# Kernel optimization log

Measured on AMD Instinct MI355X. Metric: run time of the kernel, lower is better.

Reference implementation:

```python
import jax, jax.numpy as jnp
import numpy as np

N = 50000
E = 500000
IN_C = 128
HEADS = 4
OUT_C = 64
EDGE_DIM = 32
NEG_SLOPE = 0.2  # PyG GATv2Conv default


def setup_inputs() -> dict:
    key = jax.random.key(0)
    ks = jax.random.split(key, 10)
    x = jax.random.normal(ks[0], (N, IN_C), dtype=jnp.float32)
    edge_index = jax.random.randint(ks[1], (2, E), 0, N, dtype=jnp.int64)
    edge_attr = jax.random.normal(ks[2], (E, EDGE_DIM), dtype=jnp.float32)
    s = 1.0 / np.sqrt(IN_C)
    W_l = jax.random.normal(ks[3], (IN_C, HEADS * OUT_C), dtype=jnp.float32) * s
    b_l = jnp.zeros((HEADS * OUT_C,), dtype=jnp.float32)
    W_r = jax.random.normal(ks[4], (IN_C, HEADS * OUT_C), dtype=jnp.float32) * s
    b_r = jnp.zeros((HEADS * OUT_C,), dtype=jnp.float32)
    W_e = jax.random.normal(ks[5], (EDGE_DIM, HEADS * OUT_C), dtype=jnp.float32) / np.sqrt(EDGE_DIM)
    att = jax.random.normal(ks[6], (HEADS, OUT_C), dtype=jnp.float32) / np.sqrt(OUT_C)
    bias = jnp.zeros((OUT_C,), dtype=jnp.float32)
    return {"x": x, "edge_index": edge_index, "edge_attr": edge_attr,
            "W_l": W_l, "b_l": b_l, "W_r": W_r, "b_r": b_r,
            "W_e": W_e, "att": att, "bias": bias}


def reference(x, edge_index, edge_attr, W_l, b_l, W_r, b_r, W_e, att, bias):
    # GATv2Conv forward (eval mode: dropout inactive), concat=False -> mean over heads
    src, dst = edge_index[0], edge_index[1]  # edge j -> i (source_to_target)
    x_l = (x @ W_l + b_l).reshape(N, HEADS, OUT_C)  # source transform
    x_r = (x @ W_r + b_r).reshape(N, HEADS, OUT_C)  # target transform
    e = (edge_attr @ W_e).reshape(E, HEADS, OUT_C)
    # per-edge score: att . LeakyReLU(x_l[j] + x_r[i] + e)
    m = x_l[src] + x_r[dst] + e                      # [E, H, C]
    m = jnp.where(m > 0, m, NEG_SLOPE * m)
    alpha = jnp.einsum('ehc,hc->eh', m, att)         # [E, H]
    # softmax over incoming edges of each target node
    amax = jax.ops.segment_max(alpha, dst, num_segments=N)   # [N, H]
    alpha = jnp.exp(alpha - amax[dst])
    denom = jax.ops.segment_sum(alpha, dst, num_segments=N)  # [N, H]
    alpha = alpha / denom[dst]
    # scatter-add weighted source messages
    out = jax.ops.segment_sum(alpha[:, :, None] * x_l[src], dst, num_segments=N)  # [N, H, C]
    out = out.mean(axis=1) + bias                    # concat=False -> mean heads
    return out
```

## Files before the change

kernel.cpp:

```cpp
#include <hip/hip_runtime.h>
#include <cstddef>

#define Nn 50000
#define Ee 500000
#define INC 128
#define HC 256
#define OUTC 64
#define EDIM 32
#define NEG 0.2f
#define NB 196
#define GEMMB 782

typedef __attribute__((ext_vector_type(8))) short short8;
typedef __attribute__((ext_vector_type(4))) float f32x4;

__device__ __forceinline__ unsigned short f2bf(float f) {
    unsigned u = __float_as_uint(f);
    return (unsigned short)((u + 0x7FFFu + ((u >> 16) & 1u)) >> 16);
}
__device__ __forceinline__ float bf2f(unsigned short v) {
    return __uint_as_float(((unsigned)v) << 16);
}

__device__ __forceinline__ float row_sum16(float x) {
    int i;
    i = __builtin_amdgcn_mov_dpp(__float_as_int(x), 0xB1, 0xF, 0xF, true);
    x += __int_as_float(i);
    i = __builtin_amdgcn_mov_dpp(__float_as_int(x), 0x4E, 0xF, 0xF, true);
    x += __int_as_float(i);
    i = __builtin_amdgcn_mov_dpp(__float_as_int(x), 0x141, 0xF, 0xF, true);
    x += __int_as_float(i);
    i = __builtin_amdgcn_mov_dpp(__float_as_int(x), 0x140, 0xF, 0xF, true);
    x += __int_as_float(i);
    return x;
}

__global__ __launch_bounds__(256) void pack_kernel(
    const float* __restrict__ Wl, const float* __restrict__ Wr,
    const float* __restrict__ We,
    unsigned short* __restrict__ wlf, unsigned short* __restrict__ wrf,
    unsigned short* __restrict__ wef, int* __restrict__ deg)
{
    int sid = blockIdx.x * 256 + threadIdx.x;
    if (sid >= 9216) {
        int i = sid - 9216;
        if (i < Nn) deg[i] = 0;
        return;
    }
    const float* W; unsigned short* dst; int s; int col; int k0;
    if (sid < 8192) {
        if (sid < 4096) { W = Wl; dst = wlf; s = sid; }
        else            { W = Wr; dst = wrf; s = sid - 4096; }
        int lane = s & 63;
        int T    = (s >> 6) & 15;
        int kc   = s >> 10;
        col = (lane & 15) * 16 + T;
        k0  = kc * 32 + (lane >> 4) * 8;
    } else {
        W = We; dst = wef; s = sid - 8192;
        int lane = s & 63;
        int nt   = (s >> 6) & 3;
        int cb   = s >> 8;
        col = cb * 64 + (lane & 15) * 4 + nt;
        k0  = (lane >> 4) * 8;
    }
    unsigned short tmp[8];
    #pragma unroll
    for (int j = 0; j < 8; ++j) tmp[j] = f2bf(W[(size_t)(k0 + j) * HC + col]);
    *(uint4*)(dst + (size_t)s * 8) = *(uint4*)tmp;
}

__global__ __launch_bounds__(256) void gemm_hist_kernel(
    const float* __restrict__ X,
    const unsigned short* __restrict__ wlf, const float* __restrict__ bl,
    const unsigned short* __restrict__ wrf, const float* __restrict__ br,
    unsigned short* __restrict__ Ylb, unsigned short* __restrict__ Yrb,
    const int* __restrict__ ei, int* __restrict__ deg)
{
    if (blockIdx.x >= GEMMB) {
        int e = (blockIdx.x - GEMMB) * 256 + threadIdx.x;
        if (e < Ee) atomicAdd(deg + ei[Ee + e], 1);
        return;
    }

    const int tid = threadIdx.x, lane = tid & 63;
    const int l15 = lane & 15, l4 = lane >> 4;
    const int r0 = blockIdx.x * 64 + (tid >> 6) * 16;

    int arow = r0 + l15; if (arow >= Nn) arow = Nn - 1;
    short8 af[4];
    #pragma unroll
    for (int kc = 0; kc < 4; ++kc) {
        const f32x4* p = (const f32x4*)(X + (size_t)arow * INC + kc * 32 + l4 * 8);
        f32x4 v0 = p[0], v1 = p[1];
        short8 a;
        a[0]=(short)f2bf(v0.x); a[1]=(short)f2bf(v0.y); a[2]=(short)f2bf(v0.z); a[3]=(short)f2bf(v0.w);
        a[4]=(short)f2bf(v1.x); a[5]=(short)f2bf(v1.y); a[6]=(short)f2bf(v1.z); a[7]=(short)f2bf(v1.w);
        af[kc] = a;
    }

    #pragma unroll 1
    for (int w = 0; w < 2; ++w) {
        const unsigned short* wf = w ? wrf : wlf;
        const float* b = w ? br : bl;
        unsigned short* Yb = w ? Yrb : Ylb;

        f32x4 acc[16];
        #pragma unroll
        for (int T = 0; T < 16; ++T) acc[T] = (f32x4){0.f, 0.f, 0.f, 0.f};

        #pragma unroll
        for (int kc = 0; kc < 4; ++kc) {
            #pragma unroll
            for (int T = 0; T < 16; ++T) {
                short8 bf = *(const short8*)(wf + ((size_t)(kc * 16 + T) * 64 + lane) * 8);
                acc[T] = __builtin_amdgcn_mfma_f32_16x16x32_bf16(af[kc], bf, acc[T], 0, 0, 0);
            }
        }

        float bb[16];
        #pragma unroll
        for (int t4 = 0; t4 < 4; ++t4) {
            float4 v = *(const float4*)(b + l15 * 16 + t4 * 4);
            bb[t4*4+0]=v.x; bb[t4*4+1]=v.y; bb[t4*4+2]=v.z; bb[t4*4+3]=v.w;
        }

        #pragma unroll
        for (int r = 0; r < 4; ++r) {
            int orow = r0 + l4 * 4 + r;
            if (orow < Nn) {
                unsigned short o[16];
                #pragma unroll
                for (int T = 0; T < 16; ++T) o[T] = f2bf(acc[T][r] + bb[T]);
                *(uint4*)(Yb + (size_t)orow * HC + l15 * 16)     = *(uint4*)(o);
                *(uint4*)(Yb + (size_t)orow * HC + l15 * 16 + 8) = *(uint4*)(o + 8);
            }
        }
    }
}

__global__ __launch_bounds__(256) void scan1_kernel(
    const int* __restrict__ deg, int* __restrict__ off, int* __restrict__ bsum) {
    __shared__ int s[256];
    int i = blockIdx.x * 256 + threadIdx.x;
    int v = (i < Nn) ? deg[i] : 0;
    s[threadIdx.x] = v;
    __syncthreads();
    #pragma unroll
    for (int d = 1; d < 256; d <<= 1) {
        int t = (threadIdx.x >= d) ? s[threadIdx.x - d] : 0;
        __syncthreads();
        s[threadIdx.x] += t;
        __syncthreads();
    }
    if (i < Nn) off[i] = s[threadIdx.x] - v;
    if (threadIdx.x == 255) bsum[blockIdx.x] = s[255];
}
__global__ __launch_bounds__(256) void scan3_kernel(
    int* __restrict__ off, const int* __restrict__ bsum, int* __restrict__ cur) {
    __shared__ int s[256];
    int t = threadIdx.x;
    int v = (t < NB) ? bsum[t] : 0;
    s[t] = v;
    __syncthreads();
    #pragma unroll
    for (int d = 1; d < 256; d <<= 1) {
        int tv = (t >= d) ? s[t - d] : 0;
        __syncthreads();
        s[t] += tv;
        __syncthreads();
    }
    int base = (blockIdx.x == 0) ? 0 : s[blockIdx.x - 1];
    int i = blockIdx.x * 256 + t;
    if (i < Nn) {
        int o = off[i] + base;
        off[i] = o;
        cur[i] = o;
    }
}
__global__ __launch_bounds__(256) void scatter_kernel(
    const int* __restrict__ ei, int* __restrict__ cur,
    int* __restrict__ csr_e, int* __restrict__ csr_s, int* __restrict__ csr_d) {
    int e = blockIdx.x * 256 + threadIdx.x;
    if (e >= Ee) return;
    int d = ei[Ee + e];
    int pos = atomicAdd(cur + d, 1);
    csr_e[pos] = e;
    csr_s[pos] = ei[e];
    csr_d[pos] = d;
}

__global__ __launch_bounds__(256) void edge_alpha_kernel(
    const unsigned short* __restrict__ xlb, const unsigned short* __restrict__ xrb,
    const int* __restrict__ csr_e, const int* __restrict__ csr_s,
    const int* __restrict__ csr_d, const float* __restrict__ ea,
    const unsigned short* __restrict__ wef, const float* __restrict__ att,
    float* __restrict__ alpha)
{
    const int tid  = threadIdx.x;
    const int lane = tid & 63;
    const int l15  = lane & 15, l4 = lane >> 4;
    const int p0   = blockIdx.x * 64 + (tid >> 6) * 16;

    short8 afrag;
    {
        int p = p0 + l15;
        if (p >= Ee) p = Ee - 1;
        int e = csr_e[p];
        const f32x4* pp = (const f32x4*)(ea + (size_t)e * EDIM + l4 * 8);
        f32x4 v0 = __builtin_nontemporal_load(pp);
        f32x4 v1 = __builtin_nontemporal_load(pp + 1);
        afrag[0]=(short)f2bf(v0.x); afrag[1]=(short)f2bf(v0.y);
        afrag[2]=(short)f2bf(v0.z); afrag[3]=(short)f2bf(v0.w);
        afrag[4]=(short)f2bf(v1.x); afrag[5]=(short)f2bf(v1.y);
        afrag[6]=(short)f2bf(v1.z); afrag[7]=(short)f2bf(v1.w);
    }

    unsigned soff[4], doff[4];
    #pragma unroll
    for (int r = 0; r < 4; ++r) {
        int p = p0 + l4 * 4 + r;
        int pc = (p < Ee) ? p : Ee - 1;
        soff[r] = (unsigned)csr_s[pc] * (unsigned)HC;
        doff[r] = (unsigned)csr_d[pc] * (unsigned)HC;
    }

    #pragma unroll 1
    for (int cb = 0; cb < 4; ++cb) {
        f32x4 acc[4];
        const f32x4 z = {0.f, 0.f, 0.f, 0.f};
        #pragma unroll
        for (int nt = 0; nt < 4; ++nt) {
            short8 bfrag = *(const short8*)(wef + ((size_t)(cb * 4 + nt) * 64 + lane) * 8);
            acc[nt] = __builtin_amdgcn_mfma_f32_16x16x32_bf16(afrag, bfrag, z, 0, 0, 0);
        }

        float4 atv = *(const float4*)(att + cb * 64 + l15 * 4);

        #pragma unroll
        for (int r = 0; r < 4; ++r) {
            const unsigned c = (unsigned)(cb * 64 + l15 * 4);
            ushort4 gl4 = *(const ushort4*)(xlb + soff[r] + c);
            ushort4 gr4 = *(const ushort4*)(xrb + doff[r] + c);
            float m0 = acc[0][r] + bf2f(gl4.x) + bf2f(gr4.x);
            float m1 = acc[1][r] + bf2f(gl4.y) + bf2f(gr4.y);
            float m2 = acc[2][r] + bf2f(gl4.z) + bf2f(gr4.z);
            float m3 = acc[3][r] + bf2f(gl4.w) + bf2f(gr4.w);
            m0 = fmaxf(m0, NEG * m0);
            m1 = fmaxf(m1, NEG * m1);
            m2 = fmaxf(m2, NEG * m2);
            m3 = fmaxf(m3, NEG * m3);
            float p;
            p = atv.x * m0;
            p = fmaf(atv.y, m1, p);
            p = fmaf(atv.z, m2, p);
            p = fmaf(atv.w, m3, p);
            p = row_sum16(p);
            int pp = p0 + l4 * 4 + r;
            if (l15 == 0 && pp < Ee)
                alpha[(size_t)pp * 4 + cb] = p;
        }
    }
}

__global__ __launch_bounds__(256) void node_aggr_kernel(
    const unsigned short* __restrict__ xlb,
    const int* __restrict__ csr_s,
    const float* __restrict__ alpha, const int* __restrict__ off,
    const int* __restrict__ deg, const float* __restrict__ bias,
    float* __restrict__ out)
{
    __shared__ float shw[4][64];
    __shared__ int   shs[4][16];
    const int lane = threadIdx.x & 63;
    const int wv   = threadIdx.x >> 6;
    const int n    = blockIdx.x * 4 + wv;
    if (n >= Nn) return;

    const int start = off[n];
    const int len   = deg[n];

    if (len == 0) {
        if (lane < 16) {
            float4 b4 = *(const float4*)(bias + lane * 4);
            *(float4*)(out + (size_t)n * OUTC + lane * 4) = b4;
        }
        return;
    }

    const int eidx = lane >> 2;
    const int hagg = lane >> 4;

    float m = -3.4e38f, d = 0.f;
    float4 acc = make_float4(0.f, 0.f, 0.f, 0.f);

    for (int c0 = 0; c0 < len; c0 += 16) {
        int cl = len - c0; if (cl > 16) cl = 16;
        float a = (eidx < cl) ? alpha[(size_t)(start + c0) * 4 + lane] : -3.4e38f;
        if (lane < cl) shs[wv][lane] = csr_s[start + c0 + lane];
        float cm = a;
        cm = fmaxf(cm, __shfl_xor(cm, 4, 64));
        cm = fmaxf(cm, __shfl_xor(cm, 8, 64));
        cm = fmaxf(cm, __shfl_xor(cm, 16, 64));
        cm = fmaxf(cm, __shfl_xor(cm, 32, 64));
        float mn = fmaxf(m, cm);
        float sc = __expf(m - mn);
        float w  = (eidx < cl) ? __expf(a - mn) : 0.f;
        float ws = w;
        ws += __shfl_xor(ws, 4, 64);
        ws += __shfl_xor(ws, 8, 64);
        ws += __shfl_xor(ws, 16, 64);
        ws += __shfl_xor(ws, 32, 64);
        d = d * sc + ws;
        m = mn;
        shw[wv][lane] = w;
        float sca = __shfl(sc, hagg, 64);
        acc.x *= sca; acc.y *= sca; acc.z *= sca; acc.w *= sca;
        #pragma unroll 4
        for (int i = 0; i < cl; ++i) {
            int   si = shs[wv][i];
            float wi = shw[wv][i * 4 + hagg];
            ushort4 g = *(const ushort4*)(xlb + (size_t)si * HC + lane * 4);
            acc.x = fmaf(wi, bf2f(g.x), acc.x);
            acc.y = fmaf(wi, bf2f(g.y), acc.y);
            acc.z = fmaf(wi, bf2f(g.z), acc.z);
            acc.w = fmaf(wi, bf2f(g.w), acc.w);
        }
    }

    float dh = __shfl(d, hagg, 64);
    float di = 1.f / dh;
    float4 r;
    r.x = acc.x * di; r.y = acc.y * di; r.z = acc.z * di; r.w = acc.w * di;
    r.x += __shfl_xor(r.x, 16, 64); r.y += __shfl_xor(r.y, 16, 64);
    r.z += __shfl_xor(r.z, 16, 64); r.w += __shfl_xor(r.w, 16, 64);
    r.x += __shfl_xor(r.x, 32, 64); r.y += __shfl_xor(r.y, 32, 64);
    r.z += __shfl_xor(r.z, 32, 64); r.w += __shfl_xor(r.w, 32, 64);
    if (lane < 16) {
        float4 b4 = *(const float4*)(bias + lane * 4);
        float4 o = make_float4(b4.x + 0.25f * r.x, b4.y + 0.25f * r.y,
                               b4.z + 0.25f * r.z, b4.w + 0.25f * r.w);
        *(float4*)(out + (size_t)n * OUTC + lane * 4) = o;
    }
}

extern "C" void kernel_launch(void* const* d_in, const int* in_sizes, int n_in,
                              void* d_out, int out_size, void* d_ws, size_t ws_size,
                              hipStream_t stream)
{
    const float* x    = (const float*)d_in[0];
    const int*   ei   = (const int*)d_in[1];
    const float* ea   = (const float*)d_in[2];
    const float* Wl   = (const float*)d_in[3];
    const float* bl   = (const float*)d_in[4];
    const float* Wr   = (const float*)d_in[5];
    const float* br   = (const float*)d_in[6];
    const float* We   = (const float*)d_in[7];
    const float* att  = (const float*)d_in[8];
    const float* bias = (const float*)d_in[9];
    float* out = (float*)d_out;

    unsigned short* xlb   = (unsigned short*)d_ws;
    unsigned short* xrb   = xlb + (size_t)Nn * HC;
    float*          alpha = (float*)(xrb + (size_t)Nn * HC);
    unsigned short* wef   = (unsigned short*)(alpha + (size_t)Ee * 4);
    unsigned short* wlf   = wef + 8192;
    unsigned short* wrf   = wlf + 32768;
    int*            deg   = (int*)(wrf + 32768);
    int*            off   = deg + Nn;
    int*            cur   = off + Nn;
    int*            bsum  = cur + Nn;
    int*            csr_e = bsum + 256;
    int*            csr_s = csr_e + Ee;
    int*            csr_d = csr_s + Ee;

    pack_kernel<<<232, 256, 0, stream>>>(Wl, Wr, We, wlf, wrf, wef, deg);
    gemm_hist_kernel<<<GEMMB + (Ee + 255) / 256, 256, 0, stream>>>(
        x, wlf, bl, wrf, br, xlb, xrb, ei, deg);
    scan1_kernel<<<NB, 256, 0, stream>>>(deg, off, bsum);
    scan3_kernel<<<NB, 256, 0, stream>>>(off, bsum, cur);
    scatter_kernel<<<(Ee + 255) / 256, 256, 0, stream>>>(ei, cur, csr_e, csr_s, csr_d);
    edge_alpha_kernel<<<(Ee + 63) / 64, 256, 0, stream>>>(xlb, xrb, csr_e, csr_s, csr_d, ea, wef, att, alpha);
    node_aggr_kernel<<<(Nn + 3) / 4, 256, 0, stream>>>(xlb, csr_s, alpha, off, deg, bias, out);
}
```

Measured before the change: 208.1 us.

## Fuse edge attention scoring into per-node aggregation kernel with LDS-cached source rows

Merges the edge-score kernel into the node aggregation kernel. Each wave computes attention scores for 16 incoming edges of its node with MFMA, keeps each node's x_r row in registers, and caches the gathered x_l rows in LDS so the weighted sum reuses them instead of gathering again. This drops the alpha buffer round trip, the csr_d array and one kernel launch. In exchange, MFMA work now runs per node in chunks that are partially empty for low-degree nodes, and the 32KB of LDS per block may lower occupancy.

After: 257.0 us. 1.23x slower.

```diff
diff --git a/kernel.cpp b/kernel.cpp
--- a/kernel.cpp
+++ b/kernel.cpp
@@ -180,100 +180,29 @@
 }
 __global__ __launch_bounds__(256) void scatter_kernel(
     const int* __restrict__ ei, int* __restrict__ cur,
-    int* __restrict__ csr_e, int* __restrict__ csr_s, int* __restrict__ csr_d) {
+    int* __restrict__ csr_e, int* __restrict__ csr_s) {
     int e = blockIdx.x * 256 + threadIdx.x;
     if (e >= Ee) return;
     int d = ei[Ee + e];
     int pos = atomicAdd(cur + d, 1);
     csr_e[pos] = e;
     csr_s[pos] = ei[e];
-    csr_d[pos] = d;
-}
-
-__global__ __launch_bounds__(256) void edge_alpha_kernel(
+}
+
+__global__ __launch_bounds__(256) void fused_node_kernel(
     const unsigned short* __restrict__ xlb, const unsigned short* __restrict__ xrb,
     const int* __restrict__ csr_e, const int* __restrict__ csr_s,
-    const int* __restrict__ csr_d, const float* __restrict__ ea,
-    const unsigned short* __restrict__ wef, const float* __restrict__ att,
-    float* __restrict__ alpha)
-{
-    const int tid  = threadIdx.x;
-    const int lane = tid & 63;
-    const int l15  = lane & 15, l4 = lane >> 4;
-    const int p0   = blockIdx.x * 64 + (tid >> 6) * 16;
-
-    short8 afrag;
-    {
-        int p = p0 + l15;
-        if (p >= Ee) p = Ee - 1;
-        int e = csr_e[p];
-        const f32x4* pp = (const f32x4*)(ea + (size_t)e * EDIM + l4 * 8);
-        f32x4 v0 = __builtin_nontemporal_load(pp);
-        f32x4 v1 = __builtin_nontemporal_load(pp + 1);
-        afrag[0]=(short)f2bf(v0.x); afrag[1]=(short)f2bf(v0.y);
-        afrag[2]=(short)f2bf(v0.z); afrag[3]=(short)f2bf(v0.w);
-        afrag[4]=(short)f2bf(v1.x); afrag[5]=(short)f2bf(v1.y);
-        afrag[6]=(short)f2bf(v1.z); afrag[7]=(short)f2bf(v1.w);
-    }
-
-    unsigned soff[4], doff[4];
-    #pragma unroll
-    for (int r = 0; r < 4; ++r) {
-        int p = p0 + l4 * 4 + r;
-        int pc = (p < Ee) ? p : Ee - 1;
-        soff[r] = (unsigned)csr_s[pc] * (unsigned)HC;
-        doff[r] = (unsigned)csr_d[pc] * (unsigned)HC;
-    }
-
-    #pragma unroll 1
-    for (int cb = 0; cb < 4; ++cb) {
-        f32x4 acc[4];
-        const f32x4 z = {0.f, 0.f, 0.f, 0.f};
-        #pragma unroll
-        for (int nt = 0; nt < 4; ++nt) {
-            short8 bfrag = *(const short8*)(wef + ((size_t)(cb * 4 + nt) * 64 + lane) * 8);
-            acc[nt] = __builtin_amdgcn_mfma_f32_16x16x32_bf16(afrag, bfrag, z, 0, 0, 0);
-        }
-
-        float4 atv = *(const float4*)(att + cb * 64 + l15 * 4);
-
-        #pragma unroll
-        for (int r = 0; r < 4; ++r) {
-            const unsigned c = (unsigned)(cb * 64 + l15 * 4);
-            ushort4 gl4 = *(const ushort4*)(xlb + soff[r] + c);
-            ushort4 gr4 = *(const ushort4*)(xrb + doff[r] + c);
-            float m0 = acc[0][r] + bf2f(gl4.x) + bf2f(gr4.x);
-            float m1 = acc[1][r] + bf2f(gl4.y) + bf2f(gr4.y);
-            float m2 = acc[2][r] + bf2f(gl4.z) + bf2f(gr4.z);
-            float m3 = acc[3][r] + bf2f(gl4.w) + bf2f(gr4.w);
-            m0 = fmaxf(m0, NEG * m0);
-            m1 = fmaxf(m1, NEG * m1);
-            m2 = fmaxf(m2, NEG * m2);
-            m3 = fmaxf(m3, NEG * m3);
-            float p;
-            p = atv.x * m0;
-            p = fmaf(atv.y, m1, p);
-            p = fmaf(atv.z, m2, p);
-            p = fmaf(atv.w, m3, p);
-            p = row_sum16(p);
-            int pp = p0 + l4 * 4 + r;
-            if (l15 == 0 && pp < Ee)
-                alpha[(size_t)pp * 4 + cb] = p;
-        }
-    }
-}
-
-__global__ __launch_bounds__(256) void node_aggr_kernel(
-    const unsigned short* __restrict__ xlb,
-    const int* __restrict__ csr_s,
-    const float* __restrict__ alpha, const int* __restrict__ off,
+    const float* __restrict__ ea, const unsigned short* __restrict__ wef,
+    const float* __restrict__ att, const int* __restrict__ off,
     const int* __restrict__ deg, const float* __restrict__ bias,
     float* __restrict__ out)
 {
+    __shared__ unsigned short cache[4][16][256];
+    __shared__ float sAl[4][64];
     __shared__ float shw[4][64];
-    __shared__ int   shs[4][16];
     const int lane = threadIdx.x & 63;
     const int wv   = threadIdx.x >> 6;
+    const int l15  = lane & 15, l4 = lane >> 4;
     const int n    = blockIdx.x * 4 + wv;
     if (n >= Nn) return;
 
@@ -288,6 +217,7 @@
         return;
     }
 
+    const int sA   = (l15 & 3) * 4 + (l15 >> 2);
     const int eidx = lane >> 2;
     const int hagg = lane >> 4;
 
@@ -295,9 +225,72 @@
     float4 acc = make_float4(0.f, 0.f, 0.f, 0.f);
 
     for (int c0 = 0; c0 < len; c0 += 16) {
-        int cl = len - c0; if (cl > 16) cl = 16;
-        float a = (eidx < cl) ? alpha[(size_t)(start + c0) * 4 + lane] : -3.4e38f;
-        if (lane < cl) shs[wv][lane] = csr_s[start + c0 + lane];
+        const int cl   = (len - c0 < 16) ? (len - c0) : 16;
+        const int rmax = (cl + 3) >> 2;
+
+        short8 afrag;
+        {
+            int sc_ = (sA < cl) ? sA : (cl - 1);
+            int e = csr_e[start + c0 + sc_];
+            const f32x4* pp = (const f32x4*)(ea + (size_t)e * EDIM + l4 * 8);
+            f32x4 v0 = __builtin_nontemporal_load(pp);
+            f32x4 v1 = __builtin_nontemporal_load(pp + 1);
+            afrag[0]=(short)f2bf(v0.x); afrag[1]=(short)f2bf(v0.y);
+            afrag[2]=(short)f2bf(v0.z); afrag[3]=(short)f2bf(v0.w);
+            afrag[4]=(short)f2bf(v1.x); afrag[5]=(short)f2bf(v1.y);
+            afrag[6]=(short)f2bf(v1.z); afrag[7]=(short)f2bf(v1.w);
+        }
+
+        unsigned soff[4];
+        #pragma unroll
+        for (int r = 0; r < 4; ++r) {
+            int slot = r * 4 + l4;
+            int sc_ = (slot < cl) ? slot : (cl - 1);
+            soff[r] = (unsigned)csr_s[start + c0 + sc_] * (unsigned)HC;
+        }
+
+        #pragma unroll 1
+        for (int cb = 0; cb < 4; ++cb) {
+            f32x4 acc4[4];
+            const f32x4 z = {0.f, 0.f, 0.f, 0.f};
+            #pragma unroll
+            for (int nt = 0; nt < 4; ++nt) {
+                short8 bfrag = *(const short8*)(wef + ((size_t)(cb * 4 + nt) * 64 + lane) * 8);
+                acc4[nt] = __builtin_amdgcn_mfma_f32_16x16x32_bf16(afrag, bfrag, z, 0, 0, 0);
+            }
+
+            const unsigned cc = (unsigned)(cb * 64 + l15 * 4);
+            ushort4 gr4 = *(const ushort4*)(xrb + (size_t)n * HC + cc);
+            float xr0 = bf2f(gr4.x), xr1 = bf2f(gr4.y);
+            float xr2 = bf2f(gr4.z), xr3 = bf2f(gr4.w);
+            float4 atv = *(const float4*)(att + cc);
+
+            #pragma unroll
+            for (int r = 0; r < 4; ++r) {
+                if (r < rmax) {
+                    int slot = r * 4 + l4;
+                    ushort4 gl4 = *(const ushort4*)(xlb + soff[r] + cc);
+                    *(ushort4*)(&cache[wv][slot][cc]) = gl4;
+                    float m0 = acc4[0][r] + bf2f(gl4.x) + xr0;
+                    float m1 = acc4[1][r] + bf2f(gl4.y) + xr1;
+                    float m2 = acc4[2][r] + bf2f(gl4.z) + xr2;
+                    float m3 = acc4[3][r] + bf2f(gl4.w) + xr3;
+                    m0 = fmaxf(m0, NEG * m0);
+                    m1 = fmaxf(m1, NEG * m1);
+                    m2 = fmaxf(m2, NEG * m2);
+                    m3 = fmaxf(m3, NEG * m3);
+                    float p;
+                    p = atv.x * m0;
+                    p = fmaf(atv.y, m1, p);
+                    p = fmaf(atv.z, m2, p);
+                    p = fmaf(atv.w, m3, p);
+                    p = row_sum16(p);
+                    if (l15 == 0) sAl[wv][slot * 4 + cb] = p;
+                }
+            }
+        }
+
+        float a = (eidx < cl) ? sAl[wv][lane] : -3.4e38f;
         float cm = a;
         cm = fmaxf(cm, __shfl_xor(cm, 4, 64));
         cm = fmaxf(cm, __shfl_xor(cm, 8, 64));
@@ -318,9 +311,8 @@
         acc.x *= sca; acc.y *= sca; acc.z *= sca; acc.w *= sca;
         #pragma unroll 4
         for (int i = 0; i < cl; ++i) {
-            int   si = shs[wv][i];
             float wi = shw[wv][i * 4 + hagg];
-            ushort4 g = *(const ushort4*)(xlb + (size_t)si * HC + lane * 4);
+            ushort4 g = *(const ushort4*)(&cache[wv][i][lane * 4]);
             acc.x = fmaf(wi, bf2f(g.x), acc.x);
             acc.y = fmaf(wi, bf2f(g.y), acc.y);
             acc.z = fmaf(wi, bf2f(g.z), acc.z);
@@ -362,8 +354,7 @@
 
     unsigned short* xlb   = (unsigned short*)d_ws;
     unsigned short* xrb   = xlb + (size_t)Nn * HC;
-    float*          alpha = (float*)(xrb + (size_t)Nn * HC);
-    unsigned short* wef   = (unsigned short*)(alpha + (size_t)Ee * 4);
+    unsigned short* wef   = xrb + (size_t)Nn * HC;
     unsigned short* wlf   = wef + 8192;
     unsigned short* wrf   = wlf + 32768;
     int*            deg   = (int*)(wrf + 32768);
@@ -372,14 +363,13 @@
     int*            bsum  = cur + Nn;
     int*            csr_e = bsum + 256;
     int*            csr_s = csr_e + Ee;
-    int*            csr_d = csr_s + Ee;
 
     pack_kernel<<<232, 256, 0, stream>>>(Wl, Wr, We, wlf, wrf, wef, deg);
     gemm_hist_kernel<<<GEMMB + (Ee + 255) / 256, 256, 0, stream>>>(
         x, wlf, bl, wrf, br, xlb, xrb, ei, deg);
     scan1_kernel<<<NB, 256, 0, stream>>>(deg, off, bsum);
     scan3_kernel<<<NB, 256, 0, stream>>>(off, bsum, cur);
-    scatter_kernel<<<(Ee + 255) / 256, 256, 0, stream>>>(ei, cur, csr_e, csr_s, csr_d);
-    edge_alpha_kernel<<<(Ee + 63) / 64, 256, 0, stream>>>(xlb, xrb, csr_e, csr_s, csr_d, ea, wef, att, alpha);
-    node_aggr_kernel<<<(Nn + 3) / 4, 256, 0, stream>>>(xlb, csr_s, alpha, off, deg, bias, out);
-}
+    scatter_kernel<<<(Ee + 255) / 256, 256, 0, stream>>>(ei, cur, csr_e, csr_s);
+    fused_node_kernel<<<(Nn + 3) / 4, 256, 0, stream>>>(
+        xlb, xrb, csr_e, csr_s, ea, wef, att, off, deg, bias, out);
+}
```
